# Kernel tuning notes

Hardware: AMD Instinct MI355X
Metric: run time of the kernel (lower is better)

Reference implementation:

```python
import jax, jax.numpy as jnp
import numpy as np

RADII = (1.5, 3.0)   # max radii per dilated ring
KS = (32, 64)        # neighbors per ring
OP_C = 64            # per-operator output channels
OUT_C = 256          # agg conv output channels


def setup_inputs() -> dict:
    key = jax.random.key(0)
    k = jax.random.split(key, 8)
    B, N, M, D, C = 4, 8192, 2048, 3, 64
    positions = jax.random.normal(k[0], (B, N, D), dtype=jnp.float32)
    features = jax.random.normal(k[1], (B, N, C), dtype=jnp.float32)
    centers = jax.random.normal(k[2], (B, M, D), dtype=jnp.float32)
    # squared distances in [0, 9) so both rings [1,2.25) and [2.25,9) are hit
    distances = jax.random.uniform(k[3], (B, M, N), dtype=jnp.float32) * 9.0
    W_op0 = jax.random.normal(k[4], (D + C, OP_C), dtype=jnp.float32) * 0.05
    b_op0 = jnp.zeros((OP_C,), dtype=jnp.float32)
    W_op1 = jax.random.normal(k[5], (D + C, OP_C), dtype=jnp.float32) * 0.05
    b_op1 = jnp.zeros((OP_C,), dtype=jnp.float32)
    W_agg = jax.random.normal(k[6], (2 * OP_C, OUT_C), dtype=jnp.float32) * 0.05
    b_agg = jnp.zeros((OUT_C,), dtype=jnp.float32)
    return dict(positions=positions, features=features, centers=centers,
                distances=distances, W_op0=W_op0, b_op0=b_op0,
                W_op1=W_op1, b_op1=b_op1, W_agg=W_agg, b_agg=b_agg)


def reference(positions, features, centers, distances,
              W_op0, b_op0, W_op1, b_op1, W_agg, b_agg):
    B, N, D = positions.shape
    M = centers.shape[1]
    arangeN = jnp.arange(N)
    bidx = jnp.arange(B)[:, None, None]
    min_radius = -1.0  # faithful to source: min_radius**2 == 1 in ring 0
    fs = []
    for max_radius, kk, (W, b) in zip(RADII, KS, ((W_op0, b_op0), (W_op1, b_op1))):
        excluded = (distances >= max_radius ** 2) | (distances < min_radius ** 2)
        idx = jnp.where(excluded, N, arangeN[None, None, :])   # (B,M,N)
        idx = jnp.sort(idx, axis=-1)[:, :, :kk]                # (B,M,k)
        mask = idx != N
        safe = jnp.where(mask, idx, 0)
        pos_g = positions[bidx, safe]                          # (B,M,k,D)
        feat_g = features[bidx, safe]                          # (B,M,k,C)
        rel = pos_g - centers[:, :, None, :]                   # (B,M,k,D)
        h = jax.nn.relu(jnp.concatenate([rel, feat_g], axis=-1) @ W + b)
        h = jnp.where(mask[..., None], h, 0.0)                 # invalid -> zero row
        fs.append(jnp.max(h, axis=2))                          # (B,M,OP_C)
        min_radius = max_radius
    x = jnp.concatenate(fs, axis=-1)                           # (B,M,2*OP_C)
    return jax.nn.relu(x @ W_agg + b_agg)                      # (B,M,OUT_C)
```

## Files before the change

kernel.cpp:

```cpp
#include <hip/hip_runtime.h>
#include <stdint.h>

#define BB 4
#define NN 8192
#define MM 2048
#define CC 64
#define OPC 64
#define OUTC 256
#define K0 32
#define K1 64
#define CPW 4
#define XPAD 132

typedef short bf16x8 __attribute__((ext_vector_type(8)));
typedef float f32x4  __attribute__((ext_vector_type(4)));

__device__ __forceinline__ short f2bf(float f) {
    uint32_t u = __float_as_uint(f);
    u += 0x7FFFu + ((u >> 16) & 1u);
    return (short)(u >> 16);
}

__device__ __forceinline__ uint32_t cvt_pk_bf16(float a, float b) {
    uint32_t r;
    asm("v_cvt_pk_bf16_f32 %0, %1, %2" : "=v"(r) : "v"(a), "v"(b));
    return r;
}

__device__ __forceinline__ bf16x8 pack8(float4 a, float4 b) {
    union { uint4 u; bf16x8 v; } r;
    r.u.x = cvt_pk_bf16(a.x, a.y);
    r.u.y = cvt_pk_bf16(a.z, a.w);
    r.u.z = cvt_pk_bf16(b.x, b.y);
    r.u.w = cvt_pk_bf16(b.z, b.w);
    return r.v;
}

__device__ __forceinline__ void process8(const float* dv, int base, int lane,
                                         unsigned long long lt,
                                         int* s0, int* s1,
                                         int& cnt0, int& cnt1) {
#pragma unroll
    for (int u = 0; u < 8; ++u) {
        float d = dv[u];
        bool p0 = (d >= 1.0f)  && (d < 2.25f);
        bool p1 = (d >= 2.25f) && (d < 9.0f);
        unsigned long long m0 = __ballot(p0);
        unsigned long long m1 = __ballot(p1);
        if (cnt0 < K0) {
            int pos = cnt0 + __popcll(m0 & lt);
            if (p0 && pos < K0) s0[pos] = base + u * 64 + lane;
            cnt0 += __popcll(m0);
        }
        if (cnt1 < K1) {
            int pos = cnt1 + __popcll(m1 & lt);
            if (p1 && pos < K1) s1[pos] = base + u * 64 + lane;
            cnt1 += __popcll(m1);
        }
    }
}

__global__ __launch_bounds__(256, 2) void op_kernel(
    const float* __restrict__ positions, const float* __restrict__ features,
    const float* __restrict__ centers,   const float* __restrict__ distances,
    const float* __restrict__ W0, const float* __restrict__ b0,
    const float* __restrict__ W1, const float* __restrict__ b1,
    const float* __restrict__ Wagg, const float* __restrict__ bagg,
    float* __restrict__ out)
{
    __shared__ float s_x[4][CPW][XPAD];
    __shared__ int s_idx0[4][K0];
    __shared__ int s_idx1[4][K1];

    const int w    = threadIdx.x >> 6;
    const int lane = threadIdx.x & 63;
    const int quad = lane >> 4;
    const int l15  = lane & 15;
    const int gw   = blockIdx.x * 4 + w;

    bf16x8 bfr0[3][4], bfr1[3][4];
#pragma unroll
    for (int kc = 0; kc < 3; ++kc) {
#pragma unroll
        for (int nt = 0; nt < 4; ++nt) {
            const int n = nt * 16 + l15;
            bf16x8 v0, v1;
#pragma unroll
            for (int j = 0; j < 8; ++j) {
                int k = kc * 32 + quad * 8 + j;
                float a0 = 0.f, a1 = 0.f;
                if (k < 64)      { a0 = W0[(3 + k) * OPC + n];  a1 = W1[(3 + k) * OPC + n]; }
                else if (k < 67) { a0 = W0[(k - 64) * OPC + n]; a1 = W1[(k - 64) * OPC + n]; }
                v0[j] = f2bf(a0); v1[j] = f2bf(a1);
            }
            bfr0[kc][nt] = v0; bfr1[kc][nt] = v1;
        }
    }
    float bias0v[4], bias1v[4];
#pragma unroll
    for (int nt = 0; nt < 4; ++nt) {
        bias0v[nt] = b0[nt * 16 + l15];
        bias1v[nt] = b1[nt * 16 + l15];
    }
    const unsigned long long lt = (1ull << lane) - 1ull;
    const bf16x8 zf = {0, 0, 0, 0, 0, 0, 0, 0};

    float dvp[8];
    float cxp, cyp, czp;
    {
        const float* drow0 = distances + (size_t)(gw * CPW) * NN;
#pragma unroll
        for (int u = 0; u < 8; ++u) dvp[u] = drow0[u * 64 + lane];
        cxp = centers[(size_t)(gw * CPW) * 3 + 0];
        cyp = centers[(size_t)(gw * CPW) * 3 + 1];
        czp = centers[(size_t)(gw * CPW) * 3 + 2];
    }

    for (int i = 0; i < CPW; ++i) {
        const int bm = gw * CPW + i;
        const int b  = bm >> 11;
        const float cx = cxp, cy = cyp, cz = czp;

        int cnt0 = 0, cnt1 = 0;
        process8(dvp, 0, lane, lt, s_idx0[w], s_idx1[w], cnt0, cnt1);
        if (cnt0 < K0 || cnt1 < K1) {
            const float* drow = distances + (size_t)bm * NN;
            for (int base = 512; base < NN; base += 512) {
                if (cnt0 >= K0 && cnt1 >= K1) break;
                float dv[8];
#pragma unroll
                for (int u = 0; u < 8; ++u) dv[u] = drow[base + u * 64 + lane];
                process8(dv, base, lane, lt, s_idx0[w], s_idx1[w], cnt0, cnt1);
            }
        }
        cnt0 = min(cnt0, K0);
        cnt1 = min(cnt1, K1);

        if (i + 1 < CPW) {
            const float* drn = distances + (size_t)(bm + 1) * NN;
#pragma unroll
            for (int u = 0; u < 8; ++u) dvp[u] = drn[u * 64 + lane];
            cxp = centers[(size_t)(bm + 1) * 3 + 0];
            cyp = centers[(size_t)(bm + 1) * 3 + 1];
            czp = centers[(size_t)(bm + 1) * 3 + 2];
        }

        {
            float cm[4] = {0.f, 0.f, 0.f, 0.f};
#pragma unroll
            for (int mt = 0; mt < 4; ++mt) {
                const int r = mt * 16 + l15;
                const int n = (r < cnt1) ? s_idx1[w][r] : 0;
                const float4* fb = (const float4*)(features + (size_t)((size_t)b * NN + n) * CC);
                float4 a0 = fb[quad * 2],     a1 = fb[quad * 2 + 1];
                float4 a2 = fb[8 + quad * 2], a3 = fb[8 + quad * 2 + 1];
                const float* pp = positions + (size_t)((size_t)b * NN + n) * 3;
                float rx = pp[0] - cx, ry = pp[1] - cy, rz = pp[2] - cz;
                bf16x8 af0 = pack8(a0, a1);
                bf16x8 af1 = pack8(a2, a3);
                union { uint4 u; bf16x8 v; } r2;
                r2.u.x = cvt_pk_bf16(rx, ry);
                r2.u.y = cvt_pk_bf16(rz, 0.0f);
                r2.u.z = 0u; r2.u.w = 0u;
                bf16x8 af2 = (quad == 0) ? r2.v : zf;

                f32x4 acc[4];
#pragma unroll
                for (int nt = 0; nt < 4; ++nt)
                    acc[nt] = (f32x4){bias1v[nt], bias1v[nt], bias1v[nt], bias1v[nt]};
#pragma unroll
                for (int nt = 0; nt < 4; ++nt)
                    acc[nt] = __builtin_amdgcn_mfma_f32_16x16x32_bf16(af0, bfr1[0][nt], acc[nt], 0, 0, 0);
#pragma unroll
                for (int nt = 0; nt < 4; ++nt)
                    acc[nt] = __builtin_amdgcn_mfma_f32_16x16x32_bf16(af1, bfr1[1][nt], acc[nt], 0, 0, 0);
#pragma unroll
                for (int nt = 0; nt < 4; ++nt)
                    acc[nt] = __builtin_amdgcn_mfma_f32_16x16x32_bf16(af2, bfr1[2][nt], acc[nt], 0, 0, 0);
#pragma unroll
                for (int nt = 0; nt < 4; ++nt)
#pragma unroll
                    for (int rr = 0; rr < 4; ++rr) {
                        int m = mt * 16 + quad * 4 + rr;
                        float v = (m < cnt1) ? fmaxf(acc[nt][rr], 0.f) : 0.f;
                        cm[nt] = fmaxf(cm[nt], v);
                    }
            }
#pragma unroll
            for (int nt = 0; nt < 4; ++nt) {
                cm[nt] = fmaxf(cm[nt], __shfl_xor(cm[nt], 16, 64));
                cm[nt] = fmaxf(cm[nt], __shfl_xor(cm[nt], 32, 64));
            }
            float f = (quad == 0) ? cm[0] : (quad == 1) ? cm[1]
                    : (quad == 2) ? cm[2] : cm[3];
            s_x[w][i][64 + lane] = f;
        }

        {
            float cm[4] = {0.f, 0.f, 0.f, 0.f};
#pragma unroll
            for (int mt = 0; mt < 2; ++mt) {
                const int r = mt * 16 + l15;
                const int n = (r < cnt0) ? s_idx0[w][r] : 0;
                const float4* fb = (const float4*)(features + (size_t)((size_t)b * NN + n) * CC);
                float4 a0 = fb[quad * 2],     a1 = fb[quad * 2 + 1];
                float4 a2 = fb[8 + quad * 2], a3 = fb[8 + quad * 2 + 1];
                const float* pp = positions + (size_t)((size_t)b * NN + n) * 3;
                float rx = pp[0] - cx, ry = pp[1] - cy, rz = pp[2] - cz;
                bf16x8 af0 = pack8(a0, a1);
                bf16x8 af1 = pack8(a2, a3);
                union { uint4 u; bf16x8 v; } r2;
                r2.u.x = cvt_pk_bf16(rx, ry);
                r2.u.y = cvt_pk_bf16(rz, 0.0f);
                r2.u.z = 0u; r2.u.w = 0u;
                bf16x8 af2 = (quad == 0) ? r2.v : zf;

                f32x4 acc[4];
#pragma unroll
                for (int nt = 0; nt < 4; ++nt)
                    acc[nt] = (f32x4){bias0v[nt], bias0v[nt], bias0v[nt], bias0v[nt]};
#pragma unroll
                for (int nt = 0; nt < 4; ++nt)
                    acc[nt] = __builtin_amdgcn_mfma_f32_16x16x32_bf16(af0, bfr0[0][nt], acc[nt], 0, 0, 0);
#pragma unroll
                for (int nt = 0; nt < 4; ++nt)
                    acc[nt] = __builtin_amdgcn_mfma_f32_16x16x32_bf16(af1, bfr0[1][nt], acc[nt], 0, 0, 0);
#pragma unroll
                for (int nt = 0; nt < 4; ++nt)
                    acc[nt] = __builtin_amdgcn_mfma_f32_16x16x32_bf16(af2, bfr0[2][nt], acc[nt], 0, 0, 0);
#pragma unroll
                for (int nt = 0; nt < 4; ++nt)
#pragma unroll
                    for (int rr = 0; rr < 4; ++rr) {
                        int m = mt * 16 + quad * 4 + rr;
                        float v = (m < cnt0) ? fmaxf(acc[nt][rr], 0.f) : 0.f;
                        cm[nt] = fmaxf(cm[nt], v);
                    }
            }
#pragma unroll
            for (int nt = 0; nt < 4; ++nt) {
                cm[nt] = fmaxf(cm[nt], __shfl_xor(cm[nt], 16, 64));
                cm[nt] = fmaxf(cm[nt], __shfl_xor(cm[nt], 32, 64));
            }
            float f = (quad == 0) ? cm[0] : (quad == 1) ? cm[1]
                    : (quad == 2) ? cm[2] : cm[3];
            s_x[w][i][lane] = f;
        }
    }

    __syncthreads();
    {
        const int g   = quad;
        const int j4  = w * 64 + l15 * 4;
        const int bm0 = blockIdx.x * 16;

        float4 bias4 = *(const float4*)(bagg + j4);
        f32x4 acc[4];
#pragma unroll
        for (int t = 0; t < 4; ++t)
            acc[t] = (f32x4){bias4.x, bias4.y, bias4.z, bias4.w};

#pragma unroll 2
        for (int c4 = 0; c4 < 32; ++c4) {
            float4 xq[4];
#pragma unroll
            for (int t = 0; t < 4; ++t)
                xq[t] = *(const float4*)&s_x[g][t][c4 * 4];
            float4 wv[4];
#pragma unroll
            for (int u = 0; u < 4; ++u)
                wv[u] = *(const float4*)(Wagg + (size_t)(c4 * 4 + u) * OUTC + j4);
#pragma unroll
            for (int u = 0; u < 4; ++u) {
#pragma unroll
                for (int t = 0; t < 4; ++t) {
                    const float xc = (u == 0) ? xq[t].x : (u == 1) ? xq[t].y
                                   : (u == 2) ? xq[t].z : xq[t].w;
                    acc[t][0] = fmaf(xc, wv[u].x, acc[t][0]);
                    acc[t][1] = fmaf(xc, wv[u].y, acc[t][1]);
                    acc[t][2] = fmaf(xc, wv[u].z, acc[t][2]);
                    acc[t][3] = fmaf(xc, wv[u].w, acc[t][3]);
                }
            }
        }
#pragma unroll
        for (int t = 0; t < 4; ++t) {
            float4 o = make_float4(fmaxf(acc[t][0], 0.f), fmaxf(acc[t][1], 0.f),
                                   fmaxf(acc[t][2], 0.f), fmaxf(acc[t][3], 0.f));
            *(float4*)(out + (size_t)(bm0 + g * 4 + t) * OUTC + j4) = o;
        }
    }
}

extern "C" void kernel_launch(void* const* d_in, const int* in_sizes, int n_in,
                              void* d_out, int out_size, void* d_ws, size_t ws_size,
                              hipStream_t stream) {
    const float* positions = (const float*)d_in[0];
    const float* features  = (const float*)d_in[1];
    const float* centers   = (const float*)d_in[2];
    const float* distances = (const float*)d_in[3];
    const float* W0        = (const float*)d_in[4];
    const float* b0        = (const float*)d_in[5];
    const float* W1        = (const float*)d_in[6];
    const float* b1        = (const float*)d_in[7];
    const float* Wagg      = (const float*)d_in[8];
    const float* bagg      = (const float*)d_in[9];
    float* out = (float*)d_out;
    (void)d_ws; (void)ws_size;

    op_kernel<<<512, 256, 0, stream>>>(positions, features, centers, distances,
                                       W0, b0, W1, b1, Wagg, bagg, out);
}
```

Baseline: 354.3 us.

## Stage bf16 operator weights in LDS and halve centers per wave for occupancy

Operator weight fragments are now converted to bf16 once per block by wave 0 and kept in shared memory, and each MFMA phase reloads them into registers. Before, every wave kept 24 bf16x8 fragments live in registers for the whole kernel. With that register pressure gone, launch bounds rise to 4 blocks per CU, centers per wave drop from 4 to 2, and the grid doubles to 1024 blocks. The goal is more resident waves to hide the latency of the distance scans and gathers. In exchange it adds LDS reads, a block barrier, and redundant weight conversion in every block.

After: 446.2 us. 1.26x slower.

```diff
diff --git a/kernel.cpp b/kernel.cpp
--- a/kernel.cpp
+++ b/kernel.cpp
@@ -9,7 +9,7 @@
 #define OUTC 256
 #define K0 32
 #define K1 64
-#define CPW 4
+#define CPW 2
 #define XPAD 132
 
 typedef short bf16x8 __attribute__((ext_vector_type(8)));
@@ -60,7 +60,7 @@
     }
 }
 
-__global__ __launch_bounds__(256, 2) void op_kernel(
+__global__ __launch_bounds__(256, 4) void op_kernel(
     const float* __restrict__ positions, const float* __restrict__ features,
     const float* __restrict__ centers,   const float* __restrict__ distances,
     const float* __restrict__ W0, const float* __restrict__ b0,
@@ -68,6 +68,7 @@
     const float* __restrict__ Wagg, const float* __restrict__ bagg,
     float* __restrict__ out)
 {
+    __shared__ __align__(16) short s_bfr[2][12][512];
     __shared__ float s_x[4][CPW][XPAD];
     __shared__ int s_idx0[4][K0];
     __shared__ int s_idx1[4][K1];
@@ -78,33 +79,6 @@
     const int l15  = lane & 15;
     const int gw   = blockIdx.x * 4 + w;
 
-    bf16x8 bfr0[3][4], bfr1[3][4];
-#pragma unroll
-    for (int kc = 0; kc < 3; ++kc) {
-#pragma unroll
-        for (int nt = 0; nt < 4; ++nt) {
-            const int n = nt * 16 + l15;
-            bf16x8 v0, v1;
-#pragma unroll
-            for (int j = 0; j < 8; ++j) {
-                int k = kc * 32 + quad * 8 + j;
-                float a0 = 0.f, a1 = 0.f;
-                if (k < 64)      { a0 = W0[(3 + k) * OPC + n];  a1 = W1[(3 + k) * OPC + n]; }
-                else if (k < 67) { a0 = W0[(k - 64) * OPC + n]; a1 = W1[(k - 64) * OPC + n]; }
-                v0[j] = f2bf(a0); v1[j] = f2bf(a1);
-            }
-            bfr0[kc][nt] = v0; bfr1[kc][nt] = v1;
-        }
-    }
-    float bias0v[4], bias1v[4];
-#pragma unroll
-    for (int nt = 0; nt < 4; ++nt) {
-        bias0v[nt] = b0[nt * 16 + l15];
-        bias1v[nt] = b1[nt * 16 + l15];
-    }
-    const unsigned long long lt = (1ull << lane) - 1ull;
-    const bf16x8 zf = {0, 0, 0, 0, 0, 0, 0, 0};
-
     float dvp[8];
     float cxp, cyp, czp;
     {
@@ -115,6 +89,36 @@
         cyp = centers[(size_t)(gw * CPW) * 3 + 1];
         czp = centers[(size_t)(gw * CPW) * 3 + 2];
     }
+
+    if (w == 0) {
+#pragma unroll
+        for (int kc = 0; kc < 3; ++kc) {
+#pragma unroll
+            for (int nt = 0; nt < 4; ++nt) {
+                const int n = nt * 16 + l15;
+                bf16x8 v0, v1;
+#pragma unroll
+                for (int j = 0; j < 8; ++j) {
+                    int k = kc * 32 + quad * 8 + j;
+                    float a0 = 0.f, a1 = 0.f;
+                    if (k < 64)      { a0 = W0[(3 + k) * OPC + n];  a1 = W1[(3 + k) * OPC + n]; }
+                    else if (k < 67) { a0 = W0[(k - 64) * OPC + n]; a1 = W1[(k - 64) * OPC + n]; }
+                    v0[j] = f2bf(a0); v1[j] = f2bf(a1);
+                }
+                *(bf16x8*)&s_bfr[0][kc * 4 + nt][lane * 8] = v0;
+                *(bf16x8*)&s_bfr[1][kc * 4 + nt][lane * 8] = v1;
+            }
+        }
+    }
+    float bias0v[4], bias1v[4];
+#pragma unroll
+    for (int nt = 0; nt < 4; ++nt) {
+        bias0v[nt] = b0[nt * 16 + l15];
+        bias1v[nt] = b1[nt * 16 + l15];
+    }
+    const unsigned long long lt = (1ull << lane) - 1ull;
+    const bf16x8 zf = {0, 0, 0, 0, 0, 0, 0, 0};
+    __syncthreads();
 
     for (int i = 0; i < CPW; ++i) {
         const int bm = gw * CPW + i;
@@ -146,6 +150,11 @@
         }
 
         {
+            bf16x8 bq[12];
+#pragma unroll
+            for (int q = 0; q < 12; ++q)
+                bq[q] = *(bf16x8*)&s_bfr[1][q][lane * 8];
+
             float cm[4] = {0.f, 0.f, 0.f, 0.f};
 #pragma unroll
             for (int mt = 0; mt < 4; ++mt) {
@@ -170,13 +179,13 @@
                     acc[nt] = (f32x4){bias1v[nt], bias1v[nt], bias1v[nt], bias1v[nt]};
 #pragma unroll
                 for (int nt = 0; nt < 4; ++nt)
-                    acc[nt] = __builtin_amdgcn_mfma_f32_16x16x32_bf16(af0, bfr1[0][nt], acc[nt], 0, 0, 0);
-#pragma unroll
-                for (int nt = 0; nt < 4; ++nt)
-                    acc[nt] = __builtin_amdgcn_mfma_f32_16x16x32_bf16(af1, bfr1[1][nt], acc[nt], 0, 0, 0);
-#pragma unroll
-                for (int nt = 0; nt < 4; ++nt)
-                    acc[nt] = __builtin_amdgcn_mfma_f32_16x16x32_bf16(af2, bfr1[2][nt], acc[nt], 0, 0, 0);
+                    acc[nt] = __builtin_amdgcn_mfma_f32_16x16x32_bf16(af0, bq[0 * 4 + nt], acc[nt], 0, 0, 0);
+#pragma unroll
+                for (int nt = 0; nt < 4; ++nt)
+                    acc[nt] = __builtin_amdgcn_mfma_f32_16x16x32_bf16(af1, bq[1 * 4 + nt], acc[nt], 0, 0, 0);
+#pragma unroll
+                for (int nt = 0; nt < 4; ++nt)
+                    acc[nt] = __builtin_amdgcn_mfma_f32_16x16x32_bf16(af2, bq[2 * 4 + nt], acc[nt], 0, 0, 0);
 #pragma unroll
                 for (int nt = 0; nt < 4; ++nt)
 #pragma unroll
@@ -197,6 +206,11 @@
         }
 
         {
+            bf16x8 bq[12];
+#pragma unroll
+            for (int q = 0; q < 12; ++q)
+                bq[q] = *(bf16x8*)&s_bfr[0][q][lane * 8];
+
             float cm[4] = {0.f, 0.f, 0.f, 0.f};
 #pragma unroll
             for (int mt = 0; mt < 2; ++mt) {
@@ -221,13 +235,13 @@
                     acc[nt] = (f32x4){bias0v[nt], bias0v[nt], bias0v[nt], bias0v[nt]};
 #pragma unroll
                 for (int nt = 0; nt < 4; ++nt)
-                    acc[nt] = __builtin_amdgcn_mfma_f32_16x16x32_bf16(af0, bfr0[0][nt], acc[nt], 0, 0, 0);
-#pragma unroll
-                for (int nt = 0; nt < 4; ++nt)
-                    acc[nt] = __builtin_amdgcn_mfma_f32_16x16x32_bf16(af1, bfr0[1][nt], acc[nt], 0, 0, 0);
-#pragma unroll
-                for (int nt = 0; nt < 4; ++nt)
-                    acc[nt] = __builtin_amdgcn_mfma_f32_16x16x32_bf16(af2, bfr0[2][nt], acc[nt], 0, 0, 0);
+                    acc[nt] = __builtin_amdgcn_mfma_f32_16x16x32_bf16(af0, bq[0 * 4 + nt], acc[nt], 0, 0, 0);
+#pragma unroll
+                for (int nt = 0; nt < 4; ++nt)
+                    acc[nt] = __builtin_amdgcn_mfma_f32_16x16x32_bf16(af1, bq[1 * 4 + nt], acc[nt], 0, 0, 0);
+#pragma unroll
+                for (int nt = 0; nt < 4; ++nt)
+                    acc[nt] = __builtin_amdgcn_mfma_f32_16x16x32_bf16(af2, bq[2 * 4 + nt], acc[nt], 0, 0, 0);
 #pragma unroll
                 for (int nt = 0; nt < 4; ++nt)
 #pragma unroll
@@ -252,19 +266,19 @@
     {
         const int g   = quad;
         const int j4  = w * 64 + l15 * 4;
-        const int bm0 = blockIdx.x * 16;
+        const int bm0 = blockIdx.x * (4 * CPW);
 
         float4 bias4 = *(const float4*)(bagg + j4);
-        f32x4 acc[4];
-#pragma unroll
-        for (int t = 0; t < 4; ++t)
+        f32x4 acc[CPW];
+#pragma unroll
+        for (int t = 0; t < CPW; ++t)
             acc[t] = (f32x4){bias4.x, bias4.y, bias4.z, bias4.w};
 
 #pragma unroll 2
         for (int c4 = 0; c4 < 32; ++c4) {
-            float4 xq[4];
-#pragma unroll
-            for (int t = 0; t < 4; ++t)
+            float4 xq[CPW];
+#pragma unroll
+            for (int t = 0; t < CPW; ++t)
                 xq[t] = *(const float4*)&s_x[g][t][c4 * 4];
             float4 wv[4];
 #pragma unroll
@@ -273,7 +287,7 @@
 #pragma unroll
             for (int u = 0; u < 4; ++u) {
 #pragma unroll
-                for (int t = 0; t < 4; ++t) {
+                for (int t = 0; t < CPW; ++t) {
                     const float xc = (u == 0) ? xq[t].x : (u == 1) ? xq[t].y
                                    : (u == 2) ? xq[t].z : xq[t].w;
                     acc[t][0] = fmaf(xc, wv[u].x, acc[t][0]);
@@ -284,10 +298,10 @@
             }
         }
 #pragma unroll
-        for (int t = 0; t < 4; ++t) {
+        for (int t = 0; t < CPW; ++t) {
             float4 o = make_float4(fmaxf(acc[t][0], 0.f), fmaxf(acc[t][1], 0.f),
                                    fmaxf(acc[t][2], 0.f), fmaxf(acc[t][3], 0.f));
-            *(float4*)(out + (size_t)(bm0 + g * 4 + t) * OUTC + j4) = o;
+            *(float4*)(out + (size_t)(bm0 + g * CPW + t) * OUTC + j4) = o;
         }
     }
 }
@@ -308,6 +322,6 @@
     float* out = (float*)d_out;
     (void)d_ws; (void)ws_size;
 
-    op_kernel<<<512, 256, 0, stream>>>(positions, features, centers, distances,
-                                       W0, b0, W1, b1, Wagg, bagg, out);
-}
+    op_kernel<<<1024, 256, 0, stream>>>(positions, features, centers, distances,
+                                        W0, b0, W1, b1, Wagg, bagg, out);
+}
```
